# Performance work log

Measured on AMD Instinct MI355X. Metric: run time of the kernel, lower is better.

## Reference

```python
import jax, jax.numpy as jnp
import numpy as np

MARGIN = 1.0
EPS = 1e-11


def setup_inputs() -> dict:
    key = jax.random.key(0)
    k1, k2, k3 = jax.random.split(key, 3)
    B, D, C = 8192, 512, 128
    features = jax.random.normal(k1, (B, D), dtype=jnp.float32)
    labels = jax.random.randint(k2, (B,), 0, C, dtype=jnp.int64)
    neg_u = jax.random.uniform(k3, (B,), dtype=jnp.float32)
    return {"features": features, "labels": labels, "neg_u": neg_u}


def reference(features, labels, neg_u):
    n = features.shape[0]
    sq = jnp.sum(features * features, axis=1)  # [n]
    d2 = sq[:, None] + sq[None, :] - 2.0 * (features @ features.T)
    dist = jnp.sqrt(jnp.clip(d2, EPS, None))  # [n, n]

    same = labels[:, None] == labels[None, :]
    eye = jnp.eye(n, dtype=bool)
    pos_mask = same & ~eye           # valid positives per anchor
    neg_mask = ~same                 # valid negatives per anchor
    n_neg = neg_mask.sum(axis=1)     # [n]

    # deterministic "random" negative: pick the floor(u * n_neg)-th negative
    # (stable argsort puts negatives first, preserving original order)
    order = jnp.argsort(jnp.where(neg_mask, 0, 1), axis=1, stable=True)  # [n, n]
    k = jnp.floor(neg_u * n_neg.astype(neg_u.dtype)).astype(jnp.int32)
    k = jnp.clip(k, 0, jnp.maximum(n_neg - 1, 0).astype(jnp.int32))
    neg_idx = jnp.take_along_axis(order, k[:, None], axis=1)[:, 0]       # [n]
    neg_dist = dist[jnp.arange(n), neg_idx]                               # [n]

    # MarginRankingLoss(y=1): max(0, margin + pos_dist - neg_dist), per (anchor, pos) pair
    valid = pos_mask & (n_neg > 0)[:, None]
    per_pair = jnp.maximum(MARGIN + dist - neg_dist[:, None], 0.0)
    counter = valid.sum()
    total = jnp.where(valid, per_pair, 0.0).sum()
    return total / counter.astype(total.dtype)
```

## Files before the change

### kernel.cpp

```cpp
#include <hip/hip_runtime.h>
#include <hip/hip_bf16.h>
#include <cstdint>

#define NN 8192
#define DD 512
#define NC 128

typedef unsigned short u16;
typedef __attribute__((ext_vector_type(8))) short short8;
typedef __attribute__((ext_vector_type(4))) float f32x4;

#define AS1 __attribute__((address_space(1)))
#define AS3 __attribute__((address_space(3)))

__device__ __forceinline__ float bf2f(short x) {
  return __uint_as_float(((unsigned)(unsigned short)x) << 16);
}

#define FB_OFF   ((size_t)0)
#define SQ_OFF   (FB_OFF + (size_t)NN*DD*2)
#define ND_OFF   (SQ_OFF + (size_t)NN*4)
#define ACC_OFF  (ND_OFF + (size_t)NN*4)
#define CC_OFF   (ACC_OFF + 64)
#define POS_OFF  (CC_OFF + 1024)

__global__ __launch_bounds__(256) void k_pc(const float* __restrict__ F,
    const int* __restrict__ labels, u16* __restrict__ Fb,
    float* __restrict__ sq, int* __restrict__ cc, int* __restrict__ pos) {
  const int wid = threadIdx.x >> 6, lane = threadIdx.x & 63;
  if (blockIdx.x < 2048) {
    const int row = blockIdx.x * 4 + wid;
    const float* fr = F + (size_t)row * DD + lane * 8;
    float4 v0 = *(const float4*)fr;
    float4 v1 = *(const float4*)(fr + 4);
    float s = v0.x*v0.x + v0.y*v0.y + v0.z*v0.z + v0.w*v0.w
            + v1.x*v1.x + v1.y*v1.y + v1.z*v1.z + v1.w*v1.w;
    #pragma unroll
    for (int o = 32; o; o >>= 1) s += __shfl_xor(s, o);
    float t[8] = {v0.x, v0.y, v0.z, v0.w, v1.x, v1.y, v1.z, v1.w};
    unsigned p[8];
    #pragma unroll
    for (int e = 0; e < 8; ++e) {
      unsigned b = __float_as_uint(t[e]);
      b += 0x7fffu + ((b >> 16) & 1u);
      p[e] = b >> 16;
    }
    uint4 w;
    w.x = p[0] | (p[1] << 16); w.y = p[2] | (p[3] << 16);
    w.z = p[4] | (p[5] << 16); w.w = p[6] | (p[7] << 16);
    *(uint4*)(Fb + (size_t)row * DD + lane * 8) = w;
    if (lane == 0) sq[row] = s;
  } else {
    const int c = blockIdx.x - 2048;
    __shared__ int wcnt[4], woff[4];
    const int base0 = wid * 2048;
    int cw = 0;
    for (int b = 0; b < 2048; b += 64)
      cw += __popcll(__ballot(labels[base0 + b + lane] == c));
    if (lane == 0) wcnt[wid] = cw;
    __syncthreads();
    if (threadIdx.x == 0) {
      int o = 0;
      #pragma unroll
      for (int w = 0; w < 4; ++w) { woff[w] = o; o += wcnt[w]; }
      cc[c] = o;
    }
    __syncthreads();
    int off = woff[wid];
    for (int b = 0; b < 2048; b += 64) {
      const int idx = base0 + b + lane;
      const int hit = (labels[idx] == c);
      const unsigned long long m = __ballot(hit);
      if (hit) pos[c * 128 + off + __popcll(m & ((1ull << lane) - 1ull))] = idx;
      off += __popcll(m);
    }
    __syncthreads();
    const int nc = cc[c];
    for (int t = nc + threadIdx.x; t < 128; t += 256) pos[c * 128 + t] = 0;
  }
}

__global__ __launch_bounds__(256) void k_neg2(const u16* __restrict__ Fb,
    const float* __restrict__ sq, const int* __restrict__ labels,
    const float* __restrict__ negu, const int* __restrict__ cc,
    const int* __restrict__ pos, float* __restrict__ nd,
    int* __restrict__ accz) {
  if (blockIdx.x == 0 && threadIdx.x < 16) accz[threadIdx.x] = 0;
  const int wid = threadIdx.x >> 6, lane = threadIdx.x & 63;
  const int i = blockIdx.x * 4 + wid;
  const int c = labels[i];
  const int nc = cc[c];
  const int n_neg = NN - nc;
  if (n_neg <= 0) { if (lane == 0) nd[i] = __builtin_inff(); return; }
  int k = (int)floorf(negu[i] * (float)n_neg);
  k = k < 0 ? 0 : (k > n_neg - 1 ? n_neg - 1 : k);
  const int* pc = pos + c * 128;
  const int p0 = pc[lane], p1 = pc[64 + lane];
  const int t = __popcll(__ballot((lane < nc) && (p0 - lane <= k)))
              + __popcll(__ballot((64 + lane < nc) && (p1 - (64 + lane) <= k)));
  const int j = k + t;
  const short8 av = *(const short8*)(Fb + (size_t)i * DD + lane * 8);
  const short8 bv = *(const short8*)(Fb + (size_t)j * DD + lane * 8);
  float d = 0.0f;
  #pragma unroll
  for (int e = 0; e < 8; ++e) d += bf2f(av[e]) * bf2f(bv[e]);
  #pragma unroll
  for (int o = 32; o; o >>= 1) d += __shfl_xor(d, o);
  if (lane == 0) nd[i] = sqrtf(fmaxf(sq[i] + sq[j] - 2.0f * d, 1e-11f));
}

__global__ __launch_bounds__(256) void k_cls(const u16* __restrict__ Fb,
    const float* __restrict__ sq, const float* __restrict__ nd,
    const int* __restrict__ cc, const int* __restrict__ pos,
    float* __restrict__ accf, float* __restrict__ out) {
  const int c = blockIdx.x;
  __shared__ __align__(16) u16 P[128 * 512];
  __shared__ int posc[128];
  __shared__ float red[4];
  const int tid = threadIdx.x, wid = tid >> 6, lane = tid & 63;
  const int nc = cc[c];
  if (tid < 128) posc[tid] = pos[c * 128 + tid];
  __syncthreads();
  if (nc >= 2) {
    const int wr = wid >> 1, wc = wid & 1;
    const int r16 = lane & 15, gg = lane >> 4;
    const char* fb = (const char*)Fb;

    #pragma unroll 8
    for (int s = 0; s < 32; ++s) {
      const int row = wid * 32 + s;
      const int gr = posc[row];
      __builtin_amdgcn_global_load_lds(
          (const AS1 void*)(fb + (size_t)gr * 1024 + ((lane ^ (s & 7)) << 4)),
          (AS3 void*)(&P[row * 512]), 16, 0, 0);
    }

    f32x4 acc[4][4];
    #pragma unroll
    for (int m = 0; m < 4; ++m)
      #pragma unroll
      for (int n = 0; n < 4; ++n)
        #pragma unroll
        for (int q = 0; q < 4; ++q) acc[m][n][q] = 0.0f;

    __syncthreads();
    #pragma unroll 4
    for (int t = 0; t < 16; ++t) {
      short8 af[4], bf[4];
      #pragma unroll
      for (int m = 0; m < 4; ++m) {
        const int row = wr * 64 + m * 16 + r16;
        const int gl = (t * 4 + gg) ^ (row & 7);
        af[m] = *(const short8*)&P[row * 512 + gl * 8];
      }
      #pragma unroll
      for (int n = 0; n < 4; ++n) {
        const int row = wc * 64 + n * 16 + r16;
        const int gl = (t * 4 + gg) ^ (row & 7);
        bf[n] = *(const short8*)&P[row * 512 + gl * 8];
      }
      #pragma unroll
      for (int m = 0; m < 4; ++m)
        #pragma unroll
        for (int n = 0; n < 4; ++n)
          acc[m][n] = __builtin_amdgcn_mfma_f32_16x16x32_bf16(af[m], bf[n], acc[m][n], 0, 0, 0);
    }

    float lsum = 0.0f;
    int njv[4], jv[4]; float sqj[4];
    #pragma unroll
    for (int n = 0; n < 4; ++n) {
      const int nj = wc * 64 + n * 16 + r16;
      njv[n] = nj; jv[n] = posc[nj]; sqj[n] = sq[jv[n]];
    }
    #pragma unroll
    for (int m = 0; m < 4; ++m) {
      #pragma unroll
      for (int q = 0; q < 4; ++q) {
        const int mi = wr * 64 + m * 16 + gg * 4 + q;
        const int i = posc[mi];
        const float sqi = sq[i], ndi = nd[i];
        const bool vi = mi < nc;
        #pragma unroll
        for (int n = 0; n < 4; ++n) {
          const float g = acc[m][n][q];
          const float dist = sqrtf(fmaxf(sqi + sqj[n] - 2.0f * g, 1e-11f));
          if (vi & (njv[n] < nc) & (mi != njv[n]))
            lsum += fmaxf(1.0f + dist - ndi, 0.0f);
        }
      }
    }
    #pragma unroll
    for (int o = 32; o; o >>= 1) lsum += __shfl_xor(lsum, o);
    if (lane == 0) red[wid] = lsum;
    __syncthreads();
    if (tid == 0) atomicAdd(accf, red[0] + red[1] + red[2] + red[3]);
  }
  if (tid == 0) {
    int* cnt  = (int*)accf + 1;
    int* done = (int*)accf + 2;
    if (nc < NN) atomicAdd(cnt, nc * (nc - 1));
    __threadfence();
    if (atomicAdd(done, 1) == NC - 1) {
      const float tot = atomicAdd(accf, 0.0f);
      const int n = atomicAdd(cnt, 0);
      out[0] = tot / (float)n;
    }
  }
}

extern "C" void kernel_launch(void* const* d_in, const int* in_sizes, int n_in,
                              void* d_out, int out_size, void* d_ws, size_t ws_size,
                              hipStream_t stream) {
  const float* F = (const float*)d_in[0];
  const int* labels = (const int*)d_in[1];
  const float* negu = (const float*)d_in[2];
  char* ws = (char*)d_ws;
  u16*   Fb    = (u16*)(ws + FB_OFF);
  float* sq    = (float*)(ws + SQ_OFF);
  float* nd    = (float*)(ws + ND_OFF);
  float* accf  = (float*)(ws + ACC_OFF);
  int*   cc    = (int*)(ws + CC_OFF);
  int*   pos   = (int*)(ws + POS_OFF);

  k_pc  <<<2048 + NC, 256, 0, stream>>>(F, labels, Fb, sq, cc, pos);
  k_neg2<<<NN / 4,    256, 0, stream>>>(Fb, sq, labels, negu, cc, pos, nd, (int*)accf);
  k_cls <<<NC,        256, 0, stream>>>(Fb, sq, nd, cc, pos, accf, (float*)d_out);
}
```

Baseline: 37.10 us.

## Fuse negative-distance computation into per-class loss kernel

```diff
diff --git a/kernel.cpp b/kernel.cpp
--- a/kernel.cpp
+++ b/kernel.cpp
@@ -19,16 +19,17 @@
 
 #define FB_OFF   ((size_t)0)
 #define SQ_OFF   (FB_OFF + (size_t)NN*DD*2)
-#define ND_OFF   (SQ_OFF + (size_t)NN*4)
-#define ACC_OFF  (ND_OFF + (size_t)NN*4)
+#define ACC_OFF  (SQ_OFF + (size_t)NN*4)
 #define CC_OFF   (ACC_OFF + 64)
 #define POS_OFF  (CC_OFF + 1024)
 
 __global__ __launch_bounds__(256) void k_pc(const float* __restrict__ F,
     const int* __restrict__ labels, u16* __restrict__ Fb,
-    float* __restrict__ sq, int* __restrict__ cc, int* __restrict__ pos) {
+    float* __restrict__ sq, int* __restrict__ cc, int* __restrict__ pos,
+    int* __restrict__ accz) {
   const int wid = threadIdx.x >> 6, lane = threadIdx.x & 63;
   if (blockIdx.x < 2048) {
+    if (blockIdx.x == 0 && threadIdx.x < 16) accz[threadIdx.x] = 0;
     const int row = blockIdx.x * 4 + wid;
     const float* fr = F + (size_t)row * DD + lane * 8;
     float4 v0 = *(const float4*)fr;
@@ -80,42 +81,14 @@
   }
 }
 
-__global__ __launch_bounds__(256) void k_neg2(const u16* __restrict__ Fb,
-    const float* __restrict__ sq, const int* __restrict__ labels,
-    const float* __restrict__ negu, const int* __restrict__ cc,
-    const int* __restrict__ pos, float* __restrict__ nd,
-    int* __restrict__ accz) {
-  if (blockIdx.x == 0 && threadIdx.x < 16) accz[threadIdx.x] = 0;
-  const int wid = threadIdx.x >> 6, lane = threadIdx.x & 63;
-  const int i = blockIdx.x * 4 + wid;
-  const int c = labels[i];
-  const int nc = cc[c];
-  const int n_neg = NN - nc;
-  if (n_neg <= 0) { if (lane == 0) nd[i] = __builtin_inff(); return; }
-  int k = (int)floorf(negu[i] * (float)n_neg);
-  k = k < 0 ? 0 : (k > n_neg - 1 ? n_neg - 1 : k);
-  const int* pc = pos + c * 128;
-  const int p0 = pc[lane], p1 = pc[64 + lane];
-  const int t = __popcll(__ballot((lane < nc) && (p0 - lane <= k)))
-              + __popcll(__ballot((64 + lane < nc) && (p1 - (64 + lane) <= k)));
-  const int j = k + t;
-  const short8 av = *(const short8*)(Fb + (size_t)i * DD + lane * 8);
-  const short8 bv = *(const short8*)(Fb + (size_t)j * DD + lane * 8);
-  float d = 0.0f;
-  #pragma unroll
-  for (int e = 0; e < 8; ++e) d += bf2f(av[e]) * bf2f(bv[e]);
-  #pragma unroll
-  for (int o = 32; o; o >>= 1) d += __shfl_xor(d, o);
-  if (lane == 0) nd[i] = sqrtf(fmaxf(sq[i] + sq[j] - 2.0f * d, 1e-11f));
-}
-
 __global__ __launch_bounds__(256) void k_cls(const u16* __restrict__ Fb,
-    const float* __restrict__ sq, const float* __restrict__ nd,
+    const float* __restrict__ sq, const float* __restrict__ negu,
     const int* __restrict__ cc, const int* __restrict__ pos,
     float* __restrict__ accf, float* __restrict__ out) {
   const int c = blockIdx.x;
   __shared__ __align__(16) u16 P[128 * 512];
   __shared__ int posc[128];
+  __shared__ float sqc[128], ndc[128];
   __shared__ float red[4];
   const int tid = threadIdx.x, wid = tid >> 6, lane = tid & 63;
   const int nc = cc[c];
@@ -135,6 +108,27 @@
           (AS3 void*)(&P[row * 512]), 16, 0, 0);
     }
 
+    if (tid < 128) { sqc[tid] = sq[posc[tid]]; ndc[tid] = __builtin_inff(); }
+    const int n_neg = NN - nc;
+    const int p0 = posc[lane], p1 = posc[64 + lane];
+    for (int m = wid; m < nc; m += 4) {
+      const int i = posc[m];
+      int k = (int)floorf(negu[i] * (float)n_neg);
+      k = k < 0 ? 0 : (k > n_neg - 1 ? n_neg - 1 : k);
+      const int t = __popcll(__ballot((lane < nc) && (p0 - lane <= k)))
+                  + __popcll(__ballot((64 + lane < nc) && (p1 - (64 + lane) <= k)));
+      const int j = k + t;
+      const short8 av = *(const short8*)(Fb + (size_t)i * DD + lane * 8);
+      const short8 bv = *(const short8*)(Fb + (size_t)j * DD + lane * 8);
+      float d = 0.0f;
+      #pragma unroll
+      for (int e = 0; e < 8; ++e) d += bf2f(av[e]) * bf2f(bv[e]);
+      #pragma unroll
+      for (int o = 32; o; o >>= 1) d += __shfl_xor(d, o);
+      if (lane == 0)
+        ndc[m] = sqrtf(fmaxf(sq[i] + sq[j] - 2.0f * d, 1e-11f));
+    }
+
     f32x4 acc[4][4];
     #pragma unroll
     for (int m = 0; m < 4; ++m)
@@ -167,19 +161,18 @@
     }
 
     float lsum = 0.0f;
-    int njv[4], jv[4]; float sqj[4];
+    int njv[4]; float sqj[4];
     #pragma unroll
     for (int n = 0; n < 4; ++n) {
       const int nj = wc * 64 + n * 16 + r16;
-      njv[n] = nj; jv[n] = posc[nj]; sqj[n] = sq[jv[n]];
+      njv[n] = nj; sqj[n] = sqc[nj];
     }
     #pragma unroll
     for (int m = 0; m < 4; ++m) {
       #pragma unroll
       for (int q = 0; q < 4; ++q) {
         const int mi = wr * 64 + m * 16 + gg * 4 + q;
-        const int i = posc[mi];
-        const float sqi = sq[i], ndi = nd[i];
+        const float sqi = sqc[mi], ndi = ndc[mi];
         const bool vi = mi < nc;
         #pragma unroll
         for (int n = 0; n < 4; ++n) {
@@ -218,12 +211,10 @@
   char* ws = (char*)d_ws;
   u16*   Fb    = (u16*)(ws + FB_OFF);
   float* sq    = (float*)(ws + SQ_OFF);
-  float* nd    = (float*)(ws + ND_OFF);
   float* accf  = (float*)(ws + ACC_OFF);
   int*   cc    = (int*)(ws + CC_OFF);
   int*   pos   = (int*)(ws + POS_OFF);
 
-  k_pc  <<<2048 + NC, 256, 0, stream>>>(F, labels, Fb, sq, cc, pos);
-  k_neg2<<<NN / 4,    256, 0, stream>>>(Fb, sq, labels, negu, cc, pos, nd, (int*)accf);
-  k_cls <<<NC,        256, 0, stream>>>(Fb, sq, nd, cc, pos, accf, (float*)d_out);
-}
+  k_pc <<<2048 + NC, 256, 0, stream>>>(F, labels, Fb, sq, cc, pos, (int*)accf);
+  k_cls<<<NC,        256, 0, stream>>>(Fb, sq, negu, cc, pos, accf, (float*)d_out);
+}
```

Result: slower. 48.50 us (+30.7%).
